# Optimization experiments

Hardware: AMD Instinct MI355X
Metric: run time of the kernel (lower is better)

The kernel has to match this reference:

```python
import jax, jax.numpy as jnp
import numpy as np

N, E, D, H, C = 100000, 1600000, 128, 256, 40


def setup_inputs() -> dict:
    key = jax.random.key(0)
    ks = jax.random.split(key, 10)
    x = jax.random.normal(ks[0], (N, D), dtype=jnp.float32)
    src = jax.random.randint(ks[1], (E,), 0, N, dtype=jnp.int32)
    dst = jax.random.randint(ks[2], (E,), 0, N, dtype=jnp.int32)
    # GIN layer 1 MLP (bias-free), kaiming-uniform-like scale 1/sqrt(fan_in)
    w1a = jax.random.normal(ks[3], (D, H), dtype=jnp.float32) / np.sqrt(D)
    w1b = jax.random.normal(ks[4], (H, H), dtype=jnp.float32) / np.sqrt(H)
    # GIN layer 2 MLP
    w2a = jax.random.normal(ks[5], (H, H), dtype=jnp.float32) / np.sqrt(H)
    w2b = jax.random.normal(ks[6], (H, H), dtype=jnp.float32) / np.sqrt(H)
    # eps initialized to 0 per reset_parameters
    eps1 = jnp.zeros((), dtype=jnp.float32)
    eps2 = jnp.zeros((), dtype=jnp.float32)
    # final classifier fc (with bias)
    fc_w = jax.random.normal(ks[7], (H, C), dtype=jnp.float32) / np.sqrt(H)
    fc_b = jax.random.normal(ks[8], (C,), dtype=jnp.float32) * 0.01
    return {"x": x, "src": src, "dst": dst,
            "eps1": eps1, "w1a": w1a, "w1b": w1b,
            "eps2": eps2, "w2a": w2a, "w2b": w2b,
            "fc_w": fc_w, "fc_b": fc_b}


def reference(x, src, dst, eps1, w1a, w1b, eps2, w2a, w2b, fc_w, fc_b):
    n = x.shape[0]

    def gin_layer(h, eps, wa, wb):
        # GINConv sum-aggregation: scatter-add neighbor feats over edges
        agg = jax.ops.segment_sum(h[src], dst, num_segments=n)  # [N, d]
        rst = (1.0 + eps) * h + agg
        # 2-layer bias-free MLP with ReLU between
        return jax.nn.relu(rst @ wa) @ wb

    h = jax.nn.relu(gin_layer(x, eps1, w1a, w1b))   # layer + outer activation
    h = jax.nn.relu(gin_layer(h, eps2, w2a, w2b))   # dropout p=0 -> identity
    return h @ fc_w + fc_b                           # [N, C]
```

## Files before the change

### kernel.cpp

```cpp
#include <hip/hip_runtime.h>

#define N_NODES 100000
#define N_EDGES 1600000
#define DIM_IN  128
#define DIM_H   256
#define DIM_C   40

#define NB   391
#define NBLK 391
#define CHUNK 4096
#define ECAP 6144

typedef unsigned short bf16_t;
typedef __attribute__((ext_vector_type(8))) short short8;
typedef __attribute__((ext_vector_type(4))) float f32x4;

__device__ __forceinline__ bf16_t f2b(float f) {
    unsigned int u = __float_as_uint(f);
    unsigned int r = (u + 0x7fffu + ((u >> 16) & 1u)) >> 16;
    return (bf16_t)r;
}

__device__ __forceinline__ void gl_lds16(const void* gsrc, void* ldst) {
    __builtin_amdgcn_global_load_lds(
        (const __attribute__((address_space(1))) void*)gsrc,
        (__attribute__((address_space(3))) void*)ldst,
        16, 0, 0);
}


__global__ void k_bhist(const int* __restrict__ dst, int* __restrict__ cnt2, int e) {
    __shared__ int h[NB];
    int t = threadIdx.x, blk = blockIdx.x;
    for (int i = t; i < NB; i += 256) h[i] = 0;
    __syncthreads();
    int base = blk * CHUNK;
    int end = min(base + CHUNK, e);
    for (int i = base + t; i < end; i += 256)
        atomicAdd(&h[dst[i] >> 8], 1);
    __syncthreads();
    for (int i = t; i < NB; i += 256) cnt2[blk * NB + i] = h[i];
}

__global__ void k_bscanA(const int* __restrict__ cnt2, int* __restrict__ basep,
                         int* __restrict__ btot) {
    __shared__ int s[512];
    int t = threadIdx.x, b = blockIdx.x;
    int v = (t < NBLK) ? cnt2[t * NB + b] : 0;
    s[t] = v;
    __syncthreads();
    #pragma unroll
    for (int d = 1; d < 512; d <<= 1) {
        int tv = (t >= d) ? s[t - d] : 0;
        __syncthreads();
        s[t] += tv;
        __syncthreads();
    }
    if (t < NBLK) basep[t * NB + b] = s[t] - v;
    if (t == 511) btot[b] = s[511];
}

__global__ void k_bscan2(const int* __restrict__ btot, int* __restrict__ boff) {
    __shared__ int s[512];
    int t = threadIdx.x;
    int v = (t < NB) ? btot[t] : 0;
    s[t] = v;
    __syncthreads();
    #pragma unroll
    for (int d = 1; d < 512; d <<= 1) {
        int tv = (t >= d) ? s[t - d] : 0;
        __syncthreads();
        s[t] += tv;
        __syncthreads();
    }
    if (t < NB) boff[t] = s[t] - v;
    if (t == NB - 1) boff[NB] = s[t];
}

__global__ void k_bscatter(const int* __restrict__ src, const int* __restrict__ dst,
                           const int* __restrict__ basep, const int* __restrict__ boff,
                           int* __restrict__ ebuf, int e) {
    __shared__ int cur[NB];
    int t = threadIdx.x, blk = blockIdx.x;
    for (int i = t; i < NB; i += 256) cur[i] = basep[blk * NB + i] + boff[i];
    __syncthreads();
    int base = blk * CHUNK;
    int end = min(base + CHUNK, e);
    for (int i = base + t; i < end; i += 256) {
        int sv = src[i], dv = dst[i];
        int pos = atomicAdd(&cur[dv >> 8], 1);
        ebuf[pos] = sv | ((dv & 255) << 24);
    }
}

__global__ __launch_bounds__(256) void k_build(const int* __restrict__ ebuf,
                                               const int* __restrict__ boff,
                                               int* __restrict__ off,
                                               int* __restrict__ csr) {
    __shared__ int ec[ECAP];
    __shared__ int h[256];
    __shared__ int cur[256];
    int t = threadIdx.x, b = blockIdx.x;
    int node0 = b << 8;
    int e0 = boff[b], e1 = boff[b + 1];
    int ne = e1 - e0;
    bool fits = (ne <= ECAP);
    h[t] = 0;
    __syncthreads();
    if (fits) {
        for (int i = t; i < ne; i += 256) {
            int p = ebuf[e0 + i];
            ec[i] = p;
            atomicAdd(&h[(unsigned)p >> 24], 1);
        }
    } else {
        for (int i = t; i < ne; i += 256)
            atomicAdd(&h[(unsigned)ebuf[e0 + i] >> 24], 1);
    }
    __syncthreads();
    int mydeg = h[t];
    #pragma unroll
    for (int d = 1; d < 256; d <<= 1) {
        int tv = (t >= d) ? h[t - d] : 0;
        __syncthreads();
        h[t] += tv;
        __syncthreads();
    }
    int node = node0 + t;
    if (node < N_NODES) off[node + 1] = e0 + h[t];
    if (b == 0 && t == 0) off[0] = 0;
    cur[t] = e0 + h[t] - mydeg;
    __syncthreads();
    if (fits) {
        for (int i = t; i < ne; i += 256) {
            int p = ec[i];
            int pos = atomicAdd(&cur[(unsigned)p >> 24], 1);
            csr[pos] = p & 0xFFFFFF;
        }
    } else {
        for (int i = t; i < ne; i += 256) {
            int p = ebuf[e0 + i];
            int pos = atomicAdd(&cur[(unsigned)p >> 24], 1);
            csr[pos] = p & 0xFFFFFF;
        }
    }
}


__global__ void k_cvt_i8(const float* __restrict__ x, signed char* __restrict__ x8,
                         float* __restrict__ xs, int n) {
    int gid = blockIdx.x * blockDim.x + threadIdx.x;
    int u = gid >> 6, lane = gid & 63;
    if (u >= n) return;
    float2 v = *(const float2*)(x + (size_t)u * 128 + lane * 2);
    float m = fmaxf(fabsf(v.x), fabsf(v.y));
    #pragma unroll
    for (int d = 1; d < 64; d <<= 1)
        m = fmaxf(m, __shfl_xor(m, d, 64));
    float inv = (m > 0.f) ? 127.f / m : 0.f;
    int q0 = (int)rintf(v.x * inv);
    int q1 = (int)rintf(v.y * inv);
    unsigned short pk = (unsigned short)((q0 & 0xff) | ((q1 & 0xff) << 8));
    *(unsigned short*)(x8 + ((unsigned)u << 7) + lane * 2) = pk;
    if (lane == 0) xs[u] = (m > 0.f) ? m * (1.f / 127.f) : 0.f;
}

__global__ void k_wcvt(const float* __restrict__ w1a, const float* __restrict__ w1b,
                       const float* __restrict__ w2a, const float* __restrict__ w2b,
                       const float* __restrict__ fcw,
                       bf16_t* __restrict__ o1a, bf16_t* __restrict__ o1b,
                       bf16_t* __restrict__ o2a, bf16_t* __restrict__ o2b,
                       bf16_t* __restrict__ ofc) {
    int r = blockIdx.y;
    int idx = blockIdx.x * 256 + threadIdx.x;
    const float* in; bf16_t* out; int K, N, Npad;
    switch (r) {
        case 0: in = w1a; out = o1a; K = 128; N = 256; Npad = 256; break;
        case 1: in = w1b; out = o1b; K = 256; N = 256; Npad = 256; break;
        case 2: in = w2a; out = o2a; K = 256; N = 256; Npad = 256; break;
        case 3: in = w2b; out = o2b; K = 256; N = 256; Npad = 256; break;
        default: in = fcw; out = ofc; K = 256; N = 40;  Npad = 128; break;
    }
    if (idx >= Npad * K) return;
    int n = idx / K, k = idx - n * K;
    float v = (n < N) ? in[(size_t)k * N + n] : 0.f;
    out[idx] = f2b(v);
}


__global__ void k_agg_i8(const signed char* __restrict__ h8, const float* __restrict__ hs,
                         const int* __restrict__ off, const int* __restrict__ csr,
                         const float* __restrict__ eps_p,
                         bf16_t* __restrict__ rst, int n) {
    int gid = blockIdx.x * blockDim.x + threadIdx.x;
    int u = __builtin_amdgcn_readfirstlane(gid >> 6);
    int lane = threadIdx.x & 63;
    if (u >= n) return;

    float acc0 = 0.f, acc1 = 0.f;
    int r0 = off[u], r1 = off[u + 1];
    unsigned loff = lane * 2u;

    for (int base = r0; base < r1; base += 64) {
        int m = r1 - base; if (m > 64) m = 64;
        int li = (lane < m) ? lane : (m - 1);
        int iv = csr[base + li];
        for (int c = 0; c < m; c += 16) {
            int s[16]; float sc[16]; unsigned v[16];
            #pragma unroll
            for (int t = 0; t < 16; t++)
                s[t] = __builtin_amdgcn_readlane(iv, c + t);
            #pragma unroll
            for (int t = 0; t < 16; t++)
                sc[t] = (c + t < m) ? hs[s[t]] : 0.f;
            #pragma unroll
            for (int t = 0; t < 16; t++)
                v[t] = *(const unsigned short*)(h8 + (((unsigned)s[t] << 7) + loff));
            #pragma unroll
            for (int t = 0; t < 16; t++) {
                acc0 += (float)(int)(signed char)(v[t] & 0xffu) * sc[t];
                acc1 += (float)(int)(signed char)(v[t] >> 8) * sc[t];
            }
        }
    }

    float scu = hs[u] * (1.0f + eps_p[0]);
    unsigned vu = *(const unsigned short*)(h8 + (((unsigned)u << 7) + loff));
    float o0 = (float)(int)(signed char)(vu & 0xffu) * scu + acc0;
    float o1 = (float)(int)(signed char)(vu >> 8) * scu + acc1;
    *(unsigned int*)(rst + ((unsigned)u << 7) + lane * 2) =
        (unsigned int)f2b(o0) | ((unsigned int)f2b(o1) << 16);
}


__global__ void k_agg_u8(const unsigned char* __restrict__ h8,
                         const float* __restrict__ hs,
                         const int* __restrict__ off, const int* __restrict__ csr,
                         const float* __restrict__ eps_p,
                         bf16_t* __restrict__ rst, int n) {
    int gid = blockIdx.x * blockDim.x + threadIdx.x;
    int u = __builtin_amdgcn_readfirstlane(gid >> 6);
    int lane = threadIdx.x & 63;
    if (u >= n) return;

    float acc[4] = {0.f, 0.f, 0.f, 0.f};
    int r0 = off[u], r1 = off[u + 1];
    unsigned loff = lane * 4u;

    for (int base = r0; base < r1; base += 64) {
        int m = r1 - base; if (m > 64) m = 64;
        int li = (lane < m) ? lane : (m - 1);
        int iv = csr[base + li];
        for (int c = 0; c < m; c += 16) {
            int s[16]; float sc[16]; unsigned int v[16];
            #pragma unroll
            for (int t = 0; t < 16; t++)
                s[t] = __builtin_amdgcn_readlane(iv, c + t);
            #pragma unroll
            for (int t = 0; t < 16; t++)
                sc[t] = (c + t < m) ? hs[s[t]] : 0.f;
            #pragma unroll
            for (int t = 0; t < 16; t++)
                v[t] = *(const unsigned int*)(h8 + (((unsigned)s[t] << 8) + loff));
            #pragma unroll
            for (int t = 0; t < 16; t++) {
                acc[0] += (float)(v[t] & 0xffu) * sc[t];
                acc[1] += (float)((v[t] >> 8) & 0xffu) * sc[t];
                acc[2] += (float)((v[t] >> 16) & 0xffu) * sc[t];
                acc[3] += (float)(v[t] >> 24) * sc[t];
            }
        }
    }

    float ep = 1.0f + eps_p[0];
    unsigned int vu = *(const unsigned int*)(h8 + (((unsigned)u << 8) + loff));
    float scu = hs[u] * ep;
    float o0 = (float)(vu & 0xffu) * scu + acc[0];
    float o1 = (float)((vu >> 8) & 0xffu) * scu + acc[1];
    float o2 = (float)((vu >> 16) & 0xffu) * scu + acc[2];
    float o3 = (float)(vu >> 24) * scu + acc[3];
    uint2 ov;
    ov.x = (unsigned int)f2b(o0) | ((unsigned int)f2b(o1) << 16);
    ov.y = (unsigned int)f2b(o2) | ((unsigned int)f2b(o3) << 16);
    *(uint2*)(rst + (size_t)u * 256 + lane * 4) = ov;
}


#define TS_STRIDE 264

template <int K1, bool OUT8, bool FUSE_FC>
__global__ __launch_bounds__(256, 2) void k_mlp(
    const bf16_t* __restrict__ A, const bf16_t* __restrict__ W1t,
    const bf16_t* __restrict__ W2t, bf16_t* __restrict__ H,
    unsigned char* __restrict__ H8, float* __restrict__ Hs,
    const bf16_t* __restrict__ FCt, const float* __restrict__ fc_b,
    float* __restrict__ Cout, int M)
{
    __shared__ __align__(16) bf16_t As[2][64 * 32];
    __shared__ __align__(16) bf16_t Bs[2][256 * 32];
    __shared__ __align__(16) bf16_t Ts[64 * TS_STRIDE];
    __shared__ int rmax[64];

    int tid = threadIdx.x;
    int wave = tid >> 6, lane = tid & 63;
    int l15 = lane & 15, quad = lane >> 4;
    int bm = blockIdx.x * 64;
    int wn = wave * 64;

    auto stage1 = [&](int k0, int b) {
        {
            int row = tid >> 2, k8 = (tid & 3) * 8;
            int gr = bm + row; if (gr >= M) gr = M - 1;
            gl_lds16(A + (size_t)gr * K1 + k0 + k8, &As[b][(wave * 64) * 8]);
        }
        #pragma unroll
        for (int l = 0; l < 4; l++) {
            int s = l * 256 + tid;
            int row = s >> 2, k8 = (s & 3) * 8;
            gl_lds16(W1t + (size_t)row * K1 + k0 + k8, &Bs[b][(size_t)(l * 256 + wave * 64) * 8]);
        }
    };
    auto stage2 = [&](int k0, int b) {
        #pragma unroll
        for (int l = 0; l < 4; l++) {
            int s = l * 256 + tid;
            int row = s >> 2, k8 = (s & 3) * 8;
            gl_lds16(W2t + (size_t)row * 256 + k0 + k8, &Bs[b][(size_t)(l * 256 + wave * 64) * 8]);
        }
    };

    f32x4 acc[4][4];
    #pragma unroll
    for (int i = 0; i < 4; i++)
        #pragma unroll
        for (int j = 0; j < 4; j++) acc[i][j] = 0.f;

    constexpr int NS1 = K1 / 32;
    stage1(0, 0);
    for (int k = 0; k < NS1; k++) {
        int cur = k & 1;
        if (k + 1 < NS1) {
            stage1((k + 1) * 32, cur ^ 1);
            asm volatile("s_waitcnt vmcnt(5)" ::: "memory");
        } else {
            asm volatile("s_waitcnt vmcnt(0)" ::: "memory");
        }
        __builtin_amdgcn_sched_barrier(0);
        __builtin_amdgcn_s_barrier();

        short8 af[4], bfv[4];
        #pragma unroll
        for (int i = 0; i < 4; i++)
            af[i] = *(const short8*)&As[cur][(i * 16 + l15) * 32 + quad * 8];
        #pragma unroll
        for (int j = 0; j < 4; j++)
            bfv[j] = *(const short8*)&Bs[cur][(wn + j * 16 + l15) * 32 + quad * 8];

        #pragma unroll
        for (int i = 0; i < 4; i++)
            #pragma unroll
            for (int j = 0; j < 4; j++)
                acc[i][j] = __builtin_amdgcn_mfma_f32_16x16x32_bf16(af[i], bfv[j], acc[i][j], 0, 0, 0);

        asm volatile("s_waitcnt lgkmcnt(0)" ::: "memory");
        __builtin_amdgcn_sched_barrier(0);
        __builtin_amdgcn_s_barrier();
    }

    #pragma unroll
    for (int i = 0; i < 4; i++)
        #pragma unroll
        for (int j = 0; j < 4; j++) {
            int row = i * 16 + quad * 4;
            int col = wn + j * 16 + l15;
            #pragma unroll
            for (int r = 0; r < 4; r++)
                Ts[(row + r) * TS_STRIDE + col] = f2b(fmaxf(acc[i][j][r], 0.f));
        }

    #pragma unroll
    for (int i = 0; i < 4; i++)
        #pragma unroll
        for (int j = 0; j < 4; j++) acc[i][j] = 0.f;
    __syncthreads();

    stage2(0, 0);
    for (int k = 0; k < 8; k++) {
        int cur = k & 1;
        if (k + 1 < 8) {
            stage2((k + 1) * 32, cur ^ 1);
            asm volatile("s_waitcnt vmcnt(4)" ::: "memory");
        } else {
            asm volatile("s_waitcnt vmcnt(0)" ::: "memory");
        }
        __builtin_amdgcn_sched_barrier(0);
        __builtin_amdgcn_s_barrier();

        short8 af[4], bfv[4];
        #pragma unroll
        for (int i = 0; i < 4; i++)
            af[i] = *(const short8*)&Ts[(i * 16 + l15) * TS_STRIDE + k * 32 + quad * 8];
        #pragma unroll
        for (int j = 0; j < 4; j++)
            bfv[j] = *(const short8*)&Bs[cur][(wn + j * 16 + l15) * 32 + quad * 8];

        #pragma unroll
        for (int i = 0; i < 4; i++)
            #pragma unroll
            for (int j = 0; j < 4; j++)
                acc[i][j] = __builtin_amdgcn_mfma_f32_16x16x32_bf16(af[i], bfv[j], acc[i][j], 0, 0, 0);

        asm volatile("s_waitcnt lgkmcnt(0)" ::: "memory");
        __builtin_amdgcn_sched_barrier(0);
        __builtin_amdgcn_s_barrier();
    }

    if constexpr (OUT8) {
        if (tid < 64) rmax[tid] = 0;
        __syncthreads();
        #pragma unroll
        for (int i = 0; i < 4; i++)
            #pragma unroll
            for (int r = 0; r < 4; r++) {
                float m = 0.f;
                #pragma unroll
                for (int j = 0; j < 4; j++) m = fmaxf(m, acc[i][j][r]);
                atomicMax(&rmax[i * 16 + quad * 4 + r], __float_as_int(m));
            }
        __syncthreads();
        #pragma unroll
        for (int i = 0; i < 4; i++) {
            #pragma unroll
            for (int r = 0; r < 4; r++) {
                int row = i * 16 + quad * 4 + r;
                int rowg = bm + row;
                if (rowg >= M) continue;
                float rm = __int_as_float(rmax[row]);
                float inv = (rm > 0.f) ? 255.f / rm : 0.f;
                #pragma unroll
                for (int j = 0; j < 4; j++) {
                    int col = wn + j * 16 + l15;
                    float v = fmaxf(acc[i][j][r], 0.f);
                    unsigned q = (unsigned)(v * inv + 0.5f);
                    if (q > 255u) q = 255u;
                    H8[(size_t)rowg * 256 + col] = (unsigned char)q;
                }
                if (wave == 0 && l15 == 0)
                    Hs[rowg] = rm * (1.f / 255.f);
            }
        }
    } else if constexpr (FUSE_FC) {
        #pragma unroll
        for (int i = 0; i < 4; i++)
            #pragma unroll
            for (int j = 0; j < 4; j++) {
                int row = i * 16 + quad * 4;
                int col = wn + j * 16 + l15;
                #pragma unroll
                for (int r = 0; r < 4; r++)
                    Ts[(row + r) * TS_STRIDE + col] = f2b(fmaxf(acc[i][j][r], 0.f));
            }
        __syncthreads();

        f32x4 acc3[3];
        #pragma unroll
        for (int j = 0; j < 3; j++) acc3[j] = 0.f;

        auto stage3 = [&](int k0, int b) {
            int row = tid >> 2, k8 = (tid & 3) * 8;
            gl_lds16(FCt + (size_t)row * 256 + k0 + k8, &Bs[b][(wave * 64) * 8]);
        };

        stage3(0, 0);
        for (int k = 0; k < 8; k++) {
            int cur = k & 1;
            if (k + 1 < 8) {
                stage3((k + 1) * 32, cur ^ 1);
                asm volatile("s_waitcnt vmcnt(1)" ::: "memory");
            } else {
                asm volatile("s_waitcnt vmcnt(0)" ::: "memory");
            }
            __builtin_amdgcn_sched_barrier(0);
            __builtin_amdgcn_s_barrier();

            short8 af = *(const short8*)&Ts[(wave * 16 + l15) * TS_STRIDE + k * 32 + quad * 8];
            #pragma unroll
            for (int j = 0; j < 3; j++) {
                short8 bfv = *(const short8*)&Bs[cur][(j * 16 + l15) * 32 + quad * 8];
                acc3[j] = __builtin_amdgcn_mfma_f32_16x16x32_bf16(af, bfv, acc3[j], 0, 0, 0);
            }

            asm volatile("s_waitcnt lgkmcnt(0)" ::: "memory");
            __builtin_amdgcn_sched_barrier(0);
            __builtin_amdgcn_s_barrier();
        }

        #pragma unroll
        for (int j = 0; j < 3; j++) {
            int col = j * 16 + l15;
            if (col >= DIM_C) continue;
            float bv = fc_b[col];
            #pragma unroll
            for (int r = 0; r < 4; r++) {
                int rowg = bm + wave * 16 + quad * 4 + r;
                if (rowg < M)
                    Cout[(size_t)rowg * DIM_C + col] = acc3[j][r] + bv;
            }
        }
    } else {
        #pragma unroll
        for (int j = 0; j < 4; j++) {
            int col = wn + j * 16 + l15;
            #pragma unroll
            for (int i = 0; i < 4; i++) {
                #pragma unroll
                for (int r = 0; r < 4; r++) {
                    int rowg = bm + i * 16 + quad * 4 + r;
                    if (rowg < M)
                        H[(size_t)rowg * 256 + col] = f2b(fmaxf(acc[i][j][r], 0.f));
                }
            }
        }
    }
}


static inline size_t rnd256(size_t x) { return (x + 255) & ~(size_t)255; }

extern "C" void kernel_launch(void* const* d_in, const int* in_sizes, int n_in,
                              void* d_out, int out_size, void* d_ws, size_t ws_size,
                              hipStream_t stream) {
    const float* x    = (const float*)d_in[0];
    const int*   src  = (const int*)d_in[1];
    const int*   dst  = (const int*)d_in[2];
    const float* eps1 = (const float*)d_in[3];
    const float* w1a  = (const float*)d_in[4];
    const float* w1b  = (const float*)d_in[5];
    const float* eps2 = (const float*)d_in[6];
    const float* w2a  = (const float*)d_in[7];
    const float* w2b  = (const float*)d_in[8];
    const float* fc_w = (const float*)d_in[9];
    const float* fc_b = (const float*)d_in[10];
    float* out = (float*)d_out;

    char* w = (char*)d_ws;
    int* off  = (int*)w; w += rnd256(sizeof(int) * (size_t)(N_NODES + 1));
    int* csr  = (int*)w; w += rnd256(sizeof(int) * (size_t)N_EDGES);
    int* cnt2  = (int*)w; w += rnd256(sizeof(int) * (size_t)NBLK * NB);
    int* basep = (int*)w; w += rnd256(sizeof(int) * (size_t)NBLK * NB);
    int* btot  = (int*)w; w += rnd256(sizeof(int) * 512);
    int* boff  = (int*)w; w += rnd256(sizeof(int) * (NB + 1));
    bf16_t* w1a_t = (bf16_t*)w; w += rnd256(2 * (size_t)DIM_H * DIM_IN);
    bf16_t* w1b_t = (bf16_t*)w; w += rnd256(2 * (size_t)DIM_H * DIM_H);
    bf16_t* w2a_t = (bf16_t*)w; w += rnd256(2 * (size_t)DIM_H * DIM_H);
    bf16_t* w2b_t = (bf16_t*)w; w += rnd256(2 * (size_t)DIM_H * DIM_H);
    bf16_t* fc_t  = (bf16_t*)w; w += rnd256(2 * (size_t)128 * DIM_H);
    signed char* x8 = (signed char*)w; w += rnd256((size_t)N_NODES * DIM_IN);
    float* xs = (float*)w; w += rnd256(sizeof(float) * (size_t)N_NODES);
    unsigned char* h8 = (unsigned char*)w; w += rnd256((size_t)N_NODES * DIM_H);
    float* hs = (float*)w; w += rnd256(sizeof(float) * (size_t)N_NODES);
    bf16_t* R12 = (bf16_t*)w; w += rnd256(2 * (size_t)N_NODES * DIM_H);
    bf16_t* R3  = (bf16_t*)w; w += rnd256(2 * (size_t)N_NODES * DIM_H);

    bf16_t* rst1 = R12;
    int* ebuf = (int*)R3;

    k_bhist<<<NBLK, 256, 0, stream>>>(dst, cnt2, N_EDGES);
    k_bscanA<<<NB, 512, 0, stream>>>(cnt2, basep, btot);
    k_bscan2<<<1, 512, 0, stream>>>(btot, boff);
    k_bscatter<<<NBLK, 256, 0, stream>>>(src, dst, basep, boff, ebuf, N_EDGES);
    k_build<<<NB, 256, 0, stream>>>(ebuf, boff, off, csr);

    k_cvt_i8<<<(N_NODES * 64 + 255) / 256, 256, 0, stream>>>(x, x8, xs, N_NODES);
    {
        dim3 g(256, 5);
        k_wcvt<<<g, 256, 0, stream>>>(w1a, w1b, w2a, w2b, fc_w,
                                      w1a_t, w1b_t, w2a_t, w2b_t, fc_t);
    }

    const int agg_blocks = (N_NODES * 64 + 255) / 256;
    const int mlp_blocks = (N_NODES + 63) / 64;

    k_agg_i8<<<agg_blocks, 256, 0, stream>>>(x8, xs, off, csr, eps1, rst1, N_NODES);
    k_mlp<DIM_IN, true, false><<<mlp_blocks, 256, 0, stream>>>(
        rst1, w1a_t, w1b_t, nullptr, h8, hs, nullptr, nullptr, nullptr, N_NODES);

    k_agg_u8<<<agg_blocks, 256, 0, stream>>>(h8, hs, off, csr, eps2, (bf16_t*)R3, N_NODES);
    k_mlp<DIM_H, false, true><<<mlp_blocks, 256, 0, stream>>>(
        (bf16_t*)R3, w2a_t, w2b_t, nullptr, nullptr, nullptr, fc_t, fc_b, out, N_NODES);
}
```

Measured before the change: 410.5 us.

## Fuse prep kernels, fold second scan via last-block ticket, widen MLP to 8 waves

Merges the bucket histogram, int8 feature quantization and weight transpose/convert into one launch, and folds the global bucket-offset scan into the per-bucket scan kernel using an atomic ticket so the last block finishes it. This removes three kernel launches and their gaps. The MLP kernel moves from 4 to 8 waves per block, each wave covering 32 output columns instead of 64, to raise occupancy and cut per-thread accumulator registers. The cost is extra atomics and fences in the scan, more barriers per block, and idle waves during the small FC stage.

```diff
diff --git a/kernel.cpp b/kernel.cpp
--- a/kernel.cpp
+++ b/kernel.cpp
@@ -11,6 +11,9 @@
 #define CHUNK 4096
 #define ECAP 6144
 
+#define CVT_BLOCKS 25000
+#define WCVT_BLOCKS 1280
+
 typedef unsigned short bf16_t;
 typedef __attribute__((ext_vector_type(8))) short short8;
 typedef __attribute__((ext_vector_type(4))) float f32x4;
@@ -29,22 +32,73 @@
 }
 
 
-__global__ void k_bhist(const int* __restrict__ dst, int* __restrict__ cnt2, int e) {
+__global__ __launch_bounds__(256) void k_prep(
+    const int* __restrict__ dst, int* __restrict__ cnt2,
+    const float* __restrict__ x, signed char* __restrict__ x8, float* __restrict__ xs,
+    const float* __restrict__ w1a, const float* __restrict__ w1b,
+    const float* __restrict__ w2a, const float* __restrict__ w2b,
+    const float* __restrict__ fcw,
+    bf16_t* __restrict__ o1a, bf16_t* __restrict__ o1b,
+    bf16_t* __restrict__ o2a, bf16_t* __restrict__ o2b, bf16_t* __restrict__ ofc,
+    int* __restrict__ ticket)
+{
     __shared__ int h[NB];
-    int t = threadIdx.x, blk = blockIdx.x;
-    for (int i = t; i < NB; i += 256) h[i] = 0;
-    __syncthreads();
-    int base = blk * CHUNK;
-    int end = min(base + CHUNK, e);
-    for (int i = base + t; i < end; i += 256)
-        atomicAdd(&h[dst[i] >> 8], 1);
-    __syncthreads();
-    for (int i = t; i < NB; i += 256) cnt2[blk * NB + i] = h[i];
-}
+    int blk = blockIdx.x, t = threadIdx.x;
+
+    if (blk < NBLK) {
+        if (blk == 0 && t == 0) *ticket = 0;
+        for (int i = t; i < NB; i += 256) h[i] = 0;
+        __syncthreads();
+        int base = blk * CHUNK;
+        int end = min(base + CHUNK, N_EDGES);
+        for (int i = base + t; i < end; i += 256)
+            atomicAdd(&h[dst[i] >> 8], 1);
+        __syncthreads();
+        for (int i = t; i < NB; i += 256) cnt2[blk * NB + i] = h[i];
+        return;
+    }
+    blk -= NBLK;
+
+    if (blk < CVT_BLOCKS) {
+        int gid = blk * 256 + t;
+        int u = gid >> 6, lane = gid & 63;
+        float2 v = *(const float2*)(x + (size_t)u * 128 + lane * 2);
+        float m = fmaxf(fabsf(v.x), fabsf(v.y));
+        #pragma unroll
+        for (int d = 1; d < 64; d <<= 1)
+            m = fmaxf(m, __shfl_xor(m, d, 64));
+        float inv = (m > 0.f) ? 127.f / m : 0.f;
+        int q0 = (int)rintf(v.x * inv);
+        int q1 = (int)rintf(v.y * inv);
+        unsigned short pk = (unsigned short)((q0 & 0xff) | ((q1 & 0xff) << 8));
+        *(unsigned short*)(x8 + ((unsigned)u << 7) + lane * 2) = pk;
+        if (lane == 0) xs[u] = (m > 0.f) ? m * (1.f / 127.f) : 0.f;
+        return;
+    }
+    blk -= CVT_BLOCKS;
+
+    int r = blk >> 8;
+    int idx = (blk & 255) * 256 + t;
+    const float* in; bf16_t* out; int K, N, Npad;
+    switch (r) {
+        case 0: in = w1a; out = o1a; K = 128; N = 256; Npad = 256; break;
+        case 1: in = w1b; out = o1b; K = 256; N = 256; Npad = 256; break;
+        case 2: in = w2a; out = o2a; K = 256; N = 256; Npad = 256; break;
+        case 3: in = w2b; out = o2b; K = 256; N = 256; Npad = 256; break;
+        default: in = fcw; out = ofc; K = 256; N = 40;  Npad = 128; break;
+    }
+    if (idx >= Npad * K) return;
+    int n = idx / K, k = idx - n * K;
+    float v = (n < N) ? in[(size_t)k * N + n] : 0.f;
+    out[idx] = f2b(v);
+}
+
 
 __global__ void k_bscanA(const int* __restrict__ cnt2, int* __restrict__ basep,
-                         int* __restrict__ btot) {
+                         int* __restrict__ btot, int* __restrict__ ticket,
+                         int* __restrict__ boff) {
     __shared__ int s[512];
+    __shared__ int isLast;
     int t = threadIdx.x, b = blockIdx.x;
     int v = (t < NBLK) ? cnt2[t * NB + b] : 0;
     s[t] = v;
@@ -57,14 +111,19 @@
         __syncthreads();
     }
     if (t < NBLK) basep[t * NB + b] = s[t] - v;
-    if (t == 511) btot[b] = s[511];
-}
-
-__global__ void k_bscan2(const int* __restrict__ btot, int* __restrict__ boff) {
-    __shared__ int s[512];
-    int t = threadIdx.x;
-    int v = (t < NB) ? btot[t] : 0;
-    s[t] = v;
+    if (t == 511) atomicExch(&btot[b], s[511]);
+    __syncthreads();
+    if (t == 0) {
+        __threadfence();
+        int old = atomicAdd(ticket, 1);
+        isLast = (old == NB - 1);
+    }
+    __syncthreads();
+    if (!isLast) return;
+
+    __threadfence();
+    int v2 = (t < NB) ? atomicAdd(&btot[t], 0) : 0;
+    s[t] = v2;
     __syncthreads();
     #pragma unroll
     for (int d = 1; d < 512; d <<= 1) {
@@ -73,7 +132,7 @@
         s[t] += tv;
         __syncthreads();
     }
-    if (t < NB) boff[t] = s[t] - v;
+    if (t < NB) boff[t] = s[t] - v2;
     if (t == NB - 1) boff[NB] = s[t];
 }
 
@@ -147,47 +206,6 @@
 }
 
 
-__global__ void k_cvt_i8(const float* __restrict__ x, signed char* __restrict__ x8,
-                         float* __restrict__ xs, int n) {
-    int gid = blockIdx.x * blockDim.x + threadIdx.x;
-    int u = gid >> 6, lane = gid & 63;
-    if (u >= n) return;
-    float2 v = *(const float2*)(x + (size_t)u * 128 + lane * 2);
-    float m = fmaxf(fabsf(v.x), fabsf(v.y));
-    #pragma unroll
-    for (int d = 1; d < 64; d <<= 1)
-        m = fmaxf(m, __shfl_xor(m, d, 64));
-    float inv = (m > 0.f) ? 127.f / m : 0.f;
-    int q0 = (int)rintf(v.x * inv);
-    int q1 = (int)rintf(v.y * inv);
-    unsigned short pk = (unsigned short)((q0 & 0xff) | ((q1 & 0xff) << 8));
-    *(unsigned short*)(x8 + ((unsigned)u << 7) + lane * 2) = pk;
-    if (lane == 0) xs[u] = (m > 0.f) ? m * (1.f / 127.f) : 0.f;
-}
-
-__global__ void k_wcvt(const float* __restrict__ w1a, const float* __restrict__ w1b,
-                       const float* __restrict__ w2a, const float* __restrict__ w2b,
-                       const float* __restrict__ fcw,
-                       bf16_t* __restrict__ o1a, bf16_t* __restrict__ o1b,
-                       bf16_t* __restrict__ o2a, bf16_t* __restrict__ o2b,
-                       bf16_t* __restrict__ ofc) {
-    int r = blockIdx.y;
-    int idx = blockIdx.x * 256 + threadIdx.x;
-    const float* in; bf16_t* out; int K, N, Npad;
-    switch (r) {
-        case 0: in = w1a; out = o1a; K = 128; N = 256; Npad = 256; break;
-        case 1: in = w1b; out = o1b; K = 256; N = 256; Npad = 256; break;
-        case 2: in = w2a; out = o2a; K = 256; N = 256; Npad = 256; break;
-        case 3: in = w2b; out = o2b; K = 256; N = 256; Npad = 256; break;
-        default: in = fcw; out = ofc; K = 256; N = 40;  Npad = 128; break;
-    }
-    if (idx >= Npad * K) return;
-    int n = idx / K, k = idx - n * K;
-    float v = (n < N) ? in[(size_t)k * N + n] : 0.f;
-    out[idx] = f2b(v);
-}
-
-
 __global__ void k_agg_i8(const signed char* __restrict__ h8, const float* __restrict__ hs,
                          const int* __restrict__ off, const int* __restrict__ csr,
                          const float* __restrict__ eps_p,
@@ -289,7 +307,7 @@
 #define TS_STRIDE 264
 
 template <int K1, bool OUT8, bool FUSE_FC>
-__global__ __launch_bounds__(256, 2) void k_mlp(
+__global__ __launch_bounds__(512, 4) void k_mlp(
     const bf16_t* __restrict__ A, const bf16_t* __restrict__ W1t,
     const bf16_t* __restrict__ W2t, bf16_t* __restrict__ H,
     unsigned char* __restrict__ H8, float* __restrict__ Hs,
@@ -305,35 +323,43 @@
     int wave = tid >> 6, lane = tid & 63;
     int l15 = lane & 15, quad = lane >> 4;
     int bm = blockIdx.x * 64;
-    int wn = wave * 64;
+    int wn = wave * 32;
 
     auto stage1 = [&](int k0, int b) {
-        {
+        if (tid < 256) {
             int row = tid >> 2, k8 = (tid & 3) * 8;
             int gr = bm + row; if (gr >= M) gr = M - 1;
-            gl_lds16(A + (size_t)gr * K1 + k0 + k8, &As[b][(wave * 64) * 8]);
-        }
-        #pragma unroll
-        for (int l = 0; l < 4; l++) {
-            int s = l * 256 + tid;
-            int row = s >> 2, k8 = (s & 3) * 8;
-            gl_lds16(W1t + (size_t)row * K1 + k0 + k8, &Bs[b][(size_t)(l * 256 + wave * 64) * 8]);
+            gl_lds16(A + (size_t)gr * K1 + k0 + k8, &As[b][tid * 8]);
+        }
+        {
+            int c = tid;
+            int row = c >> 2, k8 = (c & 3) * 8;
+            gl_lds16(W1t + (size_t)row * K1 + k0 + k8, &Bs[b][c * 8]);
+        }
+        {
+            int c = tid + 512;
+            int row = c >> 2, k8 = (c & 3) * 8;
+            gl_lds16(W1t + (size_t)row * K1 + k0 + k8, &Bs[b][c * 8]);
         }
     };
     auto stage2 = [&](int k0, int b) {
-        #pragma unroll
-        for (int l = 0; l < 4; l++) {
-            int s = l * 256 + tid;
-            int row = s >> 2, k8 = (s & 3) * 8;
-            gl_lds16(W2t + (size_t)row * 256 + k0 + k8, &Bs[b][(size_t)(l * 256 + wave * 64) * 8]);
+        {
+            int c = tid;
+            int row = c >> 2, k8 = (c & 3) * 8;
+            gl_lds16(W2t + (size_t)row * 256 + k0 + k8, &Bs[b][c * 8]);
+        }
+        {
+            int c = tid + 512;
+            int row = c >> 2, k8 = (c & 3) * 8;
+            gl_lds16(W2t + (size_t)row * 256 + k0 + k8, &Bs[b][c * 8]);
         }
     };
 
-    f32x4 acc[4][4];
+    f32x4 acc[4][2];
     #pragma unroll
     for (int i = 0; i < 4; i++)
         #pragma unroll
-        for (int j = 0; j < 4; j++) acc[i][j] = 0.f;
+        for (int j = 0; j < 2; j++) acc[i][j] = 0.f;
 
     constexpr int NS1 = K1 / 32;
     stage1(0, 0);
@@ -341,25 +367,26 @@
         int cur = k & 1;
         if (k + 1 < NS1) {
             stage1((k + 1) * 32, cur ^ 1);
-            asm volatile("s_waitcnt vmcnt(5)" ::: "memory");
+            if (tid < 256) { asm volatile("s_waitcnt vmcnt(3)" ::: "memory"); }
+            else           { asm volatile("s_waitcnt vmcnt(2)" ::: "memory"); }
         } else {
             asm volatile("s_waitcnt vmcnt(0)" ::: "memory");
         }
         __builtin_amdgcn_sched_barrier(0);
         __builtin_amdgcn_s_barrier();
 
-        short8 af[4], bfv[4];
+        short8 af[4], bfv[2];
         #pragma unroll
         for (int i = 0; i < 4; i++)
             af[i] = *(const short8*)&As[cur][(i * 16 + l15) * 32 + quad * 8];
         #pragma unroll
-        for (int j = 0; j < 4; j++)
+        for (int j = 0; j < 2; j++)
             bfv[j] = *(const short8*)&Bs[cur][(wn + j * 16 + l15) * 32 + quad * 8];
 
         #pragma unroll
         for (int i = 0; i < 4; i++)
             #pragma unroll
-            for (int j = 0; j < 4; j++)
+            for (int j = 0; j < 2; j++)
                 acc[i][j] = __builtin_amdgcn_mfma_f32_16x16x32_bf16(af[i], bfv[j], acc[i][j], 0, 0, 0);
 
         asm volatile("s_waitcnt lgkmcnt(0)" ::: "memory");
@@ -370,7 +397,7 @@
     #pragma unroll
     for (int i = 0; i < 4; i++)
         #pragma unroll
-        for (int j = 0; j < 4; j++) {
+        for (int j = 0; j < 2; j++) {
             int row = i * 16 + quad * 4;
             int col = wn + j * 16 + l15;
             #pragma unroll
@@ -381,7 +408,7 @@
     #pragma unroll
     for (int i = 0; i < 4; i++)
         #pragma unroll
-        for (int j = 0; j < 4; j++) acc[i][j] = 0.f;
+        for (int j = 0; j < 2; j++) acc[i][j] = 0.f;
     __syncthreads();
 
     stage2(0, 0);
@@ -389,25 +416,25 @@
         int cur = k & 1;
         if (k + 1 < 8) {
             stage2((k + 1) * 32, cur ^ 1);
-            asm volatile("s_waitcnt vmcnt(4)" ::: "memory");
+            asm volatile("s_waitcnt vmcnt(2)" ::: "memory");
         } else {
             asm volatile("s_waitcnt vmcnt(0)" ::: "memory");
         }
         __builtin_amdgcn_sched_barrier(0);
         __builtin_amdgcn_s_barrier();
 
-        short8 af[4], bfv[4];
+        short8 af[4], bfv[2];
         #pragma unroll
         for (int i = 0; i < 4; i++)
             af[i] = *(const short8*)&Ts[(i * 16 + l15) * TS_STRIDE + k * 32 + quad * 8];
         #pragma unroll
-        for (int j = 0; j < 4; j++)
+        for (int j = 0; j < 2; j++)
             bfv[j] = *(const short8*)&Bs[cur][(wn + j * 16 + l15) * 32 + quad * 8];
 
         #pragma unroll
         for (int i = 0; i < 4; i++)
             #pragma unroll
-            for (int j = 0; j < 4; j++)
+            for (int j = 0; j < 2; j++)
                 acc[i][j] = __builtin_amdgcn_mfma_f32_16x16x32_bf16(af[i], bfv[j], acc[i][j], 0, 0, 0);
 
         asm volatile("s_waitcnt lgkmcnt(0)" ::: "memory");
@@ -424,7 +451,7 @@
             for (int r = 0; r < 4; r++) {
                 float m = 0.f;
                 #pragma unroll
-                for (int j = 0; j < 4; j++) m = fmaxf(m, acc[i][j][r]);
+                for (int j = 0; j < 2; j++) m = fmaxf(m, acc[i][j][r]);
                 atomicMax(&rmax[i * 16 + quad * 4 + r], __float_as_int(m));
             }
         __syncthreads();
@@ -438,7 +465,7 @@
                 float rm = __int_as_float(rmax[row]);
                 float inv = (rm > 0.f) ? 255.f / rm : 0.f;
                 #pragma unroll
-                for (int j = 0; j < 4; j++) {
+                for (int j = 0; j < 2; j++) {
                     int col = wn + j * 16 + l15;
                     float v = fmaxf(acc[i][j][r], 0.f);
                     unsigned q = (unsigned)(v * inv + 0.5f);
@@ -453,7 +480,7 @@
         #pragma unroll
         for (int i = 0; i < 4; i++)
             #pragma unroll
-            for (int j = 0; j < 4; j++) {
+            for (int j = 0; j < 2; j++) {
                 int row = i * 16 + quad * 4;
                 int col = wn + j * 16 + l15;
                 #pragma unroll
@@ -467,8 +494,10 @@
         for (int j = 0; j < 3; j++) acc3[j] = 0.f;
 
         auto stage3 = [&](int k0, int b) {
-            int row = tid >> 2, k8 = (tid & 3) * 8;
-            gl_lds16(FCt + (size_t)row * 256 + k0 + k8, &Bs[b][(wave * 64) * 8]);
+            if (tid < 256) {
+                int row = tid >> 2, k8 = (tid & 3) * 8;
+                gl_lds16(FCt + (size_t)row * 256 + k0 + k8, &Bs[b][tid * 8]);
+            }
         };
 
         stage3(0, 0);
@@ -476,40 +505,43 @@
             int cur = k & 1;
             if (k + 1 < 8) {
                 stage3((k + 1) * 32, cur ^ 1);
-                asm volatile("s_waitcnt vmcnt(1)" ::: "memory");
+                if (tid < 256) { asm volatile("s_waitcnt vmcnt(1)" ::: "memory"); }
             } else {
-                asm volatile("s_waitcnt vmcnt(0)" ::: "memory");
+                if (tid < 256) { asm volatile("s_waitcnt vmcnt(0)" ::: "memory"); }
             }
             __builtin_amdgcn_sched_barrier(0);
             __builtin_amdgcn_s_barrier();
 
-            short8 af = *(const short8*)&Ts[(wave * 16 + l15) * TS_STRIDE + k * 32 + quad * 8];
-            #pragma unroll
-            for (int j = 0; j < 3; j++) {
-                short8 bfv = *(const short8*)&Bs[cur][(j * 16 + l15) * 32 + quad * 8];
-                acc3[j] = __builtin_amdgcn_mfma_f32_16x16x32_bf16(af, bfv, acc3[j], 0, 0, 0);
-            }
-
-            asm volatile("s_waitcnt lgkmcnt(0)" ::: "memory");
+            if (tid < 256) {
+                short8 af = *(const short8*)&Ts[(wave * 16 + l15) * TS_STRIDE + k * 32 + quad * 8];
+                #pragma unroll
+                for (int j = 0; j < 3; j++) {
+                    short8 bfv = *(const short8*)&Bs[cur][(j * 16 + l15) * 32 + quad * 8];
+                    acc3[j] = __builtin_amdgcn_mfma_f32_16x16x32_bf16(af, bfv, acc3[j], 0, 0, 0);
+                }
+                asm volatile("s_waitcnt lgkmcnt(0)" ::: "memory");
+            }
             __builtin_amdgcn_sched_barrier(0);
             __builtin_amdgcn_s_barrier();
         }
 
-        #pragma unroll
-        for (int j = 0; j < 3; j++) {
-            int col = j * 16 + l15;
-            if (col >= DIM_C) continue;
-            float bv = fc_b[col];
-            #pragma unroll
-            for (int r = 0; r < 4; r++) {
-                int rowg = bm + wave * 16 + quad * 4 + r;
-                if (rowg < M)
-                    Cout[(size_t)rowg * DIM_C + col] = acc3[j][r] + bv;
+        if (tid < 256) {
+            #pragma unroll
+            for (int j = 0; j < 3; j++) {
+                int col = j * 16 + l15;
+                if (col >= DIM_C) continue;
+                float bv = fc_b[col];
+                #pragma unroll
+                for (int r = 0; r < 4; r++) {
+                    int rowg = bm + wave * 16 + quad * 4 + r;
+                    if (rowg < M)
+                        Cout[(size_t)rowg * DIM_C + col] = acc3[j][r] + bv;
+                }
             }
         }
     } else {
         #pragma unroll
-        for (int j = 0; j < 4; j++) {
+        for (int j = 0; j < 2; j++) {
             int col = wn + j * 16 + l15;
             #pragma unroll
             for (int i = 0; i < 4; i++) {
@@ -564,28 +596,24 @@
 
     bf16_t* rst1 = R12;
     int* ebuf = (int*)R3;
-
-    k_bhist<<<NBLK, 256, 0, stream>>>(dst, cnt2, N_EDGES);
-    k_bscanA<<<NB, 512, 0, stream>>>(cnt2, basep, btot);
-    k_bscan2<<<1, 512, 0, stream>>>(btot, boff);
+    int* ticket = btot + 500;
+
+    k_prep<<<NBLK + CVT_BLOCKS + WCVT_BLOCKS, 256, 0, stream>>>(
+        dst, cnt2, x, x8, xs, w1a, w1b, w2a, w2b, fc_w,
+        w1a_t, w1b_t, w2a_t, w2b_t, fc_t, ticket);
+
+    k_bscanA<<<NB, 512, 0, stream>>>(cnt2, basep, btot, ticket, boff);
     k_bscatter<<<NBLK, 256, 0, stream>>>(src, dst, basep, boff, ebuf, N_EDGES);
     k_build<<<NB, 256, 0, stream>>>(ebuf, boff, off, csr);
 
-    k_cvt_i8<<<(N_NODES * 64 + 255) / 256, 256, 0, stream>>>(x, x8, xs, N_NODES);
-    {
-        dim3 g(256, 5);
-        k_wcvt<<<g, 256, 0, stream>>>(w1a, w1b, w2a, w2b, fc_w,
-                                      w1a_t, w1b_t, w2a_t, w2b_t, fc_t);
-    }
-
     const int agg_blocks = (N_NODES * 64 + 255) / 256;
     const int mlp_blocks = (N_NODES + 63) / 64;
 
     k_agg_i8<<<agg_blocks, 256, 0, stream>>>(x8, xs, off, csr, eps1, rst1, N_NODES);
-    k_mlp<DIM_IN, true, false><<<mlp_blocks, 256, 0, stream>>>(
+    k_mlp<DIM_IN, true, false><<<mlp_blocks, 512, 0, stream>>>(
         rst1, w1a_t, w1b_t, nullptr, h8, hs, nullptr, nullptr, nullptr, N_NODES);
 
     k_agg_u8<<<agg_blocks, 256, 0, stream>>>(h8, hs, off, csr, eps2, (bf16_t*)R3, N_NODES);
-    k_mlp<DIM_H, false, true><<<mlp_blocks, 256, 0, stream>>>(
+    k_mlp<DIM_H, false, true><<<mlp_blocks, 512, 0, stream>>>(
         (bf16_t*)R3, w2a_t, w2b_t, nullptr, nullptr, nullptr, fc_t, fc_b, out, N_NODES);
 }
```

Result: slower. 421.4 us (+2.7%).
